# Kernel tuning notes

Measured on AMD Instinct MI355X. Metric: run time of the kernel, lower is better.

## Reference

```python
import jax, jax.numpy as jnp
import numpy as np

B, T, C, H = 2, 2048, 1024, 16
D = C // H  # head dim


def setup_inputs() -> dict:
    key = jax.random.key(0)
    ks = jax.random.split(key, 8)
    s = 1.0 / np.sqrt(C)
    return {
        "x_q": jax.random.normal(ks[0], (B, T, C), jnp.float32),
        "x_kv": jax.random.normal(ks[1], (B, T, C), jnp.float32),
        "Wq": jax.random.normal(ks[2], (C, C), jnp.float32) * s,
        "bq": jnp.zeros((C,), jnp.float32),
        "Wkv": jax.random.normal(ks[3], (C, 2 * C), jnp.float32) * s,
        "bkv": jnp.zeros((2 * C,), jnp.float32),
        "Wo": jax.random.normal(ks[4], (C, C), jnp.float32) * s,
        "bo": jnp.zeros((C,), jnp.float32),
    }


def reference(x_q, x_kv, Wq, bq, Wkv, bkv, Wo, bo):
    q = x_q @ Wq + bq                      # [B,Tq,C]
    kv = x_kv @ Wkv + bkv                  # [B,Tkv,2C]
    k, v = kv[..., :C], kv[..., C:]
    # split heads -> [B,H,T,D]
    q = q.reshape(B, T, H, D).transpose(0, 2, 1, 3)
    k = k.reshape(B, T, H, D).transpose(0, 2, 1, 3)
    v = v.reshape(B, T, H, D).transpose(0, 2, 1, 3)
    att = jnp.einsum("bhqd,bhkd->bhqk", q, k) * (1.0 / np.sqrt(D))
    att = jax.nn.softmax(att, axis=-1)
    y = jnp.einsum("bhqk,bhkd->bhqd", att, v)
    y = y.transpose(0, 2, 1, 3).reshape(B, T, C)
    return y @ Wo + bo
```

## Files before the change

### kernel.cpp

```cpp
#include <hip/hip_runtime.h>

#define NB 2
#define NT 2048
#define NC 1024
#define NH 16
#define ND 64
#define NC2 2048
#define QSCALE (0.125f * 1.4426950408889634f)

typedef __attribute__((ext_vector_type(8))) __bf16 bf16x8;
typedef __attribute__((ext_vector_type(8))) unsigned short ushort8;
typedef __attribute__((ext_vector_type(4))) float f32x4;

__device__ __forceinline__ unsigned short bf16_bits(float f) {
  union { float f; unsigned int u; } x; x.f = f;
  unsigned int r = x.u + 0x7fffu + ((x.u >> 16) & 1u);
  return (unsigned short)(r >> 16);
}
__device__ __forceinline__ float bf2f(unsigned short u) {
  union { unsigned int u; float f; } x; x.u = ((unsigned int)u) << 16;
  return x.f;
}
__device__ __forceinline__ void g2l16(const void* g, void* l) {
  __builtin_amdgcn_global_load_lds(
      (const __attribute__((address_space(1))) unsigned int*)g,
      (__attribute__((address_space(3))) unsigned int*)l, 16, 0, 0);
}
__device__ __forceinline__ bf16x8 ld8(const unsigned short* p) {
  return *(const bf16x8*)p;
}
__device__ __forceinline__ unsigned int cvtpk(float lo, float hi) {
  unsigned int r;
  asm("v_cvt_pk_bf16_f32 %0, %1, %2" : "=v"(r) : "v"(lo), "v"(hi));
  return r;
}
__device__ __forceinline__ float vexp2(float x) {
  float r;
  asm("v_exp_f32 %0, %1" : "=v"(r) : "v"(x));
  return r;
}

__device__ __forceinline__ int wave_is_f32(const unsigned short* __restrict__ x) {
  const int lane = threadIdx.x & 63;
  ulonglong2 v = ((const ulonglong2*)x)[lane];
  const unsigned short* u = (const unsigned short*)&v;
  int c = 0;
#pragma unroll
  for (int k = 0; k < 8; ++k) {
    int e = (u[k] >> 7) & 0xFF;
    c += (e != 0 && (e < 112 || e > 142)) ? 1 : 0;
  }
#pragma unroll
  for (int off = 32; off > 0; off >>= 1) c += __shfl_down(c, off);
  return __shfl(c, 0) > 64;
}

__global__ __launch_bounds__(256) void prep(const void* __restrict__ xq,
                                            const void* __restrict__ xkv,
                                            const void* __restrict__ w0,
                                            const void* __restrict__ w1,
                                            const void* __restrict__ w2,
                                            unsigned short* __restrict__ oq,
                                            unsigned short* __restrict__ okv,
                                            unsigned short* __restrict__ o0,
                                            unsigned short* __restrict__ o1,
                                            unsigned short* __restrict__ o2) {
  __shared__ unsigned short tile[32][33];
  const int bx = blockIdx.x, by = blockIdx.y;
  const int f = wave_is_f32((const unsigned short*)xq);
  if (bx < 128) {
    const int fb = bx * 32 + by;
    const void* in = (fb < 2048) ? xq : xkv;
    unsigned short* out = (fb < 2048) ? oq : okv;
    const int i = (fb & 2047) * 256 + threadIdx.x;
    if (f) {
      const float4* p = (const float4*)in;
      float4 a = p[i * 2], b = p[i * 2 + 1];
      ushort8 o;
      o[0] = bf16_bits(a.x); o[1] = bf16_bits(a.y); o[2] = bf16_bits(a.z); o[3] = bf16_bits(a.w);
      o[4] = bf16_bits(b.x); o[5] = bf16_bits(b.y); o[6] = bf16_bits(b.z); o[7] = bf16_bits(b.w);
      *(ushort8*)&out[(size_t)i * 8] = o;
    } else {
      ((ulonglong2*)out)[i] = ((const ulonglong2*)in)[i];
    }
  } else {
    const int tb = bx - 128;
    const void* in; unsigned short* out; int cols, cb;
    if (tb < 32)      { in = w0; out = o0; cols = NC;  cb = tb; }
    else if (tb < 96) { in = w1; out = o1; cols = NC2; cb = tb - 32; }
    else              { in = w2; out = o2; cols = NC;  cb = tb - 96; }
    const int c0 = cb * 32, r0 = by * 32;
    const int tx = threadIdx.x & 31, ty = threadIdx.x >> 5;
#pragma unroll
    for (int i = 0; i < 32; i += 8) {
      size_t idx = (size_t)(r0 + ty + i) * cols + c0 + tx;
      tile[ty + i][tx] = f ? bf16_bits(((const float*)in)[idx]) : ((const unsigned short*)in)[idx];
    }
    __syncthreads();
#pragma unroll
    for (int i = 0; i < 32; i += 8)
      out[(size_t)(c0 + ty + i) * NC + r0 + tx] = tile[tx][ty + i];
  }
}

__global__ __launch_bounds__(256) void gemm_qkv(const unsigned short* __restrict__ xq,
                                                const unsigned short* __restrict__ xkv,
                                                const unsigned short* __restrict__ Wqt,
                                                const unsigned short* __restrict__ Wkvt,
                                                const void* __restrict__ bq,
                                                const void* __restrict__ bkv,
                                                unsigned short* __restrict__ qb,
                                                unsigned short* __restrict__ kf2,
                                                unsigned short* __restrict__ vt2,
                                                const unsigned short* __restrict__ xdet) {
  __shared__ unsigned short As[128][64];
  __shared__ unsigned short Bs[128][64];
  __shared__ unsigned short Cb[4][16][72];
  const int f = wave_is_f32(xdet);
  const int l = blockIdx.y * 32 + blockIdx.x;
  const int nl = (l & 7) * 96 + (l >> 3);
  const int bxs = nl & 31, bys = nl >> 5;
  const bool isq = bys < 8;
  const unsigned short* A  = isq ? xq : xkv;
  const unsigned short* Bt = isq ? Wqt : Wkvt;
  const int m0 = bxs * 128;
  const int n0 = (isq ? bys : bys - 8) * 128;
  const int tid = threadIdx.x, w = tid >> 6, lane = tid & 63;
  const int lrow = lane & 15, lhi = lane >> 4;
  const int wr = w >> 1, wc = w & 1;
  const int grow = lane >> 3, gcol = (lane & 7) * 8;
  f32x4 acc[4][4] = {};
  for (int k0 = 0; k0 < NC; k0 += 64) {
    __syncthreads();
#pragma unroll
    for (int p = 0; p < 4; ++p) {
      const int r = w * 32 + p * 8;
      g2l16(&A[(size_t)(m0 + r + grow) * NC + k0 + gcol], &As[r][0]);
      g2l16(&Bt[(size_t)(n0 + r + grow) * NC + k0 + gcol], &Bs[r][0]);
    }
    __syncthreads();
    bf16x8 af[2][4], bfr[2][4];
#pragma unroll
    for (int kk = 0; kk < 2; ++kk) {
#pragma unroll
      for (int i = 0; i < 4; ++i)
        af[kk][i] = ld8(&As[wr * 64 + i * 16 + lrow][kk * 32 + lhi * 8]);
#pragma unroll
      for (int j = 0; j < 4; ++j)
        bfr[kk][j] = ld8(&Bs[wc * 64 + j * 16 + lrow][kk * 32 + lhi * 8]);
    }
#pragma unroll
    for (int kk = 0; kk < 2; ++kk)
#pragma unroll
      for (int i = 0; i < 4; ++i)
#pragma unroll
        for (int j = 0; j < 4; ++j)
          acc[i][j] = __builtin_amdgcn_mfma_f32_16x16x32_bf16(af[kk][i], bfr[kk][j], acc[i][j], 0, 0, 0);
  }
  const void* bias = isq ? bq : bkv;
  if (!isq && n0 >= NC) {
#pragma unroll
    for (int j = 0; j < 4; ++j) {
      const int col = n0 + wc * 64 + j * 16 + lrow;
      const float bj = f ? ((const float*)bias)[col] : bf2f(((const unsigned short*)bias)[col]);
#pragma unroll
      for (int i = 0; i < 4; ++i) {
        const int row = m0 + wr * 64 + i * 16 + lhi * 4;
        float v[4];
#pragma unroll
        for (int r = 0; r < 4; ++r) v[r] = acc[i][j][r] + bj;
        const int cv = col - NC;
        const int hV = cv >> 6, dcol = cv & 63;
        const int bV = row >> 11, tt = row & 2047;
        const size_t base = ((size_t)((bV * NH + hV) * 32 + (tt >> 6))) * 4096
                          + (dcol >> 4) * 1024 + ((tt >> 4) & 1) * 512
                          + (((tt >> 2) & 3) * 16 + (dcol & 15)) * 8 + ((tt >> 5) & 1) * 4;
        ushort4 o4;
        o4.x = bf16_bits(v[0]); o4.y = bf16_bits(v[1]);
        o4.z = bf16_bits(v[2]); o4.w = bf16_bits(v[3]);
        *(ushort4*)&vt2[base] = o4;
      }
    }
  } else {
    const int rowbase = m0 + wr * 64;
    const int hK = (n0 + wc * 64) >> 6;
    const size_t tb = ((size_t)(((rowbase >> 11) * NH + hK) * 32 + ((rowbase & 2047) >> 6))) * 4096;
#pragma unroll
    for (int i = 0; i < 4; ++i) {
#pragma unroll
      for (int j = 0; j < 4; ++j) {
        const int col = n0 + wc * 64 + j * 16 + lrow;
        const float bj = f ? ((const float*)bias)[col] : bf2f(((const unsigned short*)bias)[col]);
#pragma unroll
        for (int r = 0; r < 4; ++r) {
          const float v = acc[i][j][r] + bj;
          Cb[w][lhi * 4 + r][j * 16 + lrow] = bf16_bits(isq ? v * QSCALE : v);
        }
      }
      if (isq) {
#pragma unroll
        for (int p = 0; p < 2; ++p) {
          const int row_l = p * 8 + (lane >> 3), col_l = (lane & 7) * 8;
          const bf16x8 v8 = ld8(&Cb[w][row_l][col_l]);
          *(bf16x8*)&qb[(size_t)(rowbase + i * 16 + row_l) * NC + n0 + wc * 64 + col_l] = v8;
        }
      } else {
#pragma unroll
        for (int p = 0; p < 2; ++p) {
          const bf16x8 v8 = ld8(&Cb[w][lane & 15][p * 32 + (lane >> 4) * 8]);
          *(bf16x8*)&kf2[tb + i * 1024 + p * 512 + lane * 8] = v8;
        }
      }
    }
  }
}

__global__ __launch_bounds__(256) void gemm_out(const unsigned short* __restrict__ A,
                                                const unsigned short* __restrict__ Bt,
                                                const void* __restrict__ bias,
                                                void* __restrict__ Cout,
                                                const unsigned short* __restrict__ xdet) {
  __shared__ unsigned short As[128][64];
  __shared__ unsigned short Bs[128][64];
  const int f = wave_is_f32(xdet);
  const int l = blockIdx.y * 32 + blockIdx.x;
  const int nl = (l & 7) * 32 + (l >> 3);
  const int m0 = (nl & 31) * 128, n0 = (nl >> 5) * 128;
  const int tid = threadIdx.x, w = tid >> 6, lane = tid & 63;
  const int lrow = lane & 15, lhi = lane >> 4;
  const int wr = w >> 1, wc = w & 1;
  const int grow = lane >> 3, gcol = (lane & 7) * 8;
  f32x4 acc[4][4] = {};
  for (int k0 = 0; k0 < NC; k0 += 64) {
    __syncthreads();
#pragma unroll
    for (int p = 0; p < 4; ++p) {
      const int r = w * 32 + p * 8;
      g2l16(&A[(size_t)(m0 + r + grow) * NC + k0 + gcol], &As[r][0]);
      g2l16(&Bt[(size_t)(n0 + r + grow) * NC + k0 + gcol], &Bs[r][0]);
    }
    __syncthreads();
    bf16x8 af[2][4], bfr[2][4];
#pragma unroll
    for (int kk = 0; kk < 2; ++kk) {
#pragma unroll
      for (int i = 0; i < 4; ++i)
        af[kk][i] = ld8(&As[wr * 64 + i * 16 + lrow][kk * 32 + lhi * 8]);
#pragma unroll
      for (int j = 0; j < 4; ++j)
        bfr[kk][j] = ld8(&Bs[wc * 64 + j * 16 + lrow][kk * 32 + lhi * 8]);
    }
#pragma unroll
    for (int kk = 0; kk < 2; ++kk)
#pragma unroll
      for (int i = 0; i < 4; ++i)
#pragma unroll
        for (int j = 0; j < 4; ++j)
          acc[i][j] = __builtin_amdgcn_mfma_f32_16x16x32_bf16(af[kk][i], bfr[kk][j], acc[i][j], 0, 0, 0);
  }
#pragma unroll
  for (int j = 0; j < 4; ++j) {
    const int col = n0 + wc * 64 + j * 16 + lrow;
    const float bj = f ? ((const float*)bias)[col] : bf2f(((const unsigned short*)bias)[col]);
#pragma unroll
    for (int i = 0; i < 4; ++i) {
      const int row = m0 + wr * 64 + i * 16 + lhi * 4;
#pragma unroll
      for (int r = 0; r < 4; ++r) {
        const float v = acc[i][j][r] + bj;
        const size_t idx = (size_t)(row + r) * NC + col;
        if (f) ((float*)Cout)[idx] = v;
        else ((unsigned short*)Cout)[idx] = bf16_bits(v);
      }
    }
  }
}

__global__ __launch_bounds__(128) void flash_attn(const unsigned short* __restrict__ q,
                                                  const unsigned short* __restrict__ kf2,
                                                  const unsigned short* __restrict__ vt2,
                                                  unsigned short* __restrict__ y) {
  const int fid = blockIdx.x + (blockIdx.y << 5);
  const int swz = ((fid & 7) << 7) + (fid >> 3);
  const int qt = swz & 31, bh = swz >> 5;
  const int b = bh >> 4, h = bh & 15;
  const int tid = threadIdx.x, w = tid >> 6, lane = tid & 63;
  const int lq = lane & 15, lhi = lane >> 4;

  bf16x8 qfA[2], qfB[2];
  {
    const unsigned short* qpA = q + (size_t)(b * NT + qt * 64 + w * 32 + lq) * NC + h * ND + lhi * 8;
    qfA[0] = ld8(qpA); qfA[1] = ld8(qpA + 32);
    qfB[0] = ld8(qpA + (size_t)16 * NC); qfB[1] = ld8(qpA + (size_t)16 * NC + 32);
  }
  f32x4 accA[4] = {}, accB[4] = {};
  float lA = 0.f, lB = 0.f;
  const unsigned short* kbase = kf2 + ((size_t)bh * 32) * 4096 + (size_t)lane * 8;
  const unsigned short* vbase = vt2 + ((size_t)bh * 32) * 4096 + (size_t)lane * 8;

#define KLOAD(kt_)                                                              \
  {                                                                             \
    _Pragma("unroll") for (int j = 0; j < 4; ++j)                               \
      _Pragma("unroll") for (int kk = 0; kk < 2; ++kk)                          \
        kR[j][kk] = ld8(kbase + (size_t)(kt_)*4096 + j * 1024 + kk * 512);      \
  }
#define VLOAD(kt_, V_)                                                          \
  {                                                                             \
    _Pragma("unroll") for (int jd = 0; jd < 4; ++jd)                            \
      _Pragma("unroll") for (int jj = 0; jj < 2; ++jj)                          \
        V_[jd][jj] = ld8(vbase + (size_t)(kt_)*4096 + jd * 1024 + jj * 512);    \
  }
#define TILE_BODY(it_, VC_, VN_)                                                  \
  {                                                                               \
    f32x4 sA[4], sB[4];                                                           \
    _Pragma("unroll") for (int j = 0; j < 4; ++j) {                               \
      f32x4 a = {}, bb2 = {};                                                     \
      _Pragma("unroll") for (int kk = 0; kk < 2; ++kk) {                          \
        a   = __builtin_amdgcn_mfma_f32_16x16x32_bf16(kR[j][kk], qfA[kk], a, 0, 0, 0);   \
        bb2 = __builtin_amdgcn_mfma_f32_16x16x32_bf16(kR[j][kk], qfB[kk], bb2, 0, 0, 0); \
      }                                                                           \
      sA[j] = a; sB[j] = bb2;                                                     \
    }                                                                             \
    if ((it_) + 1 < 32) KLOAD((it_) + 1);                                         \
    if ((it_) + 1 < 32) VLOAD((it_) + 1, VN_);                                    \
    float rsA = 0.f, rsB = 0.f;                                                   \
    _Pragma("unroll") for (int j = 0; j < 4; ++j)                                 \
      _Pragma("unroll") for (int r = 0; r < 4; ++r) {                             \
        const float pa = vexp2(sA[j][r]); sA[j][r] = pa; rsA += pa;               \
        const float pb = vexp2(sB[j][r]); sB[j][r] = pb; rsB += pb;               \
      }                                                                           \
    rsA += __shfl_xor(rsA, 16); rsA += __shfl_xor(rsA, 32);                       \
    rsB += __shfl_xor(rsB, 16); rsB += __shfl_xor(rsB, 32);                       \
    lA += rsA; lB += rsB;                                                         \
    union U { unsigned int u[4]; bf16x8 v; };                                     \
    U pA0, pA1, pB0, pB1;                                                         \
    pA0.u[0] = cvtpk(sA[0][0], sA[0][1]); pA0.u[1] = cvtpk(sA[0][2], sA[0][3]);   \
    pA0.u[2] = cvtpk(sA[2][0], sA[2][1]); pA0.u[3] = cvtpk(sA[2][2], sA[2][3]);   \
    pA1.u[0] = cvtpk(sA[1][0], sA[1][1]); pA1.u[1] = cvtpk(sA[1][2], sA[1][3]);   \
    pA1.u[2] = cvtpk(sA[3][0], sA[3][1]); pA1.u[3] = cvtpk(sA[3][2], sA[3][3]);   \
    pB0.u[0] = cvtpk(sB[0][0], sB[0][1]); pB0.u[1] = cvtpk(sB[0][2], sB[0][3]);   \
    pB0.u[2] = cvtpk(sB[2][0], sB[2][1]); pB0.u[3] = cvtpk(sB[2][2], sB[2][3]);   \
    pB1.u[0] = cvtpk(sB[1][0], sB[1][1]); pB1.u[1] = cvtpk(sB[1][2], sB[1][3]);   \
    pB1.u[2] = cvtpk(sB[3][0], sB[3][1]); pB1.u[3] = cvtpk(sB[3][2], sB[3][3]);   \
    __builtin_amdgcn_s_setprio(1);                                                \
    _Pragma("unroll") for (int jd = 0; jd < 4; ++jd) {                            \
      accA[jd] = __builtin_amdgcn_mfma_f32_16x16x32_bf16(VC_[jd][0], pA0.v, accA[jd], 0, 0, 0); \
      accA[jd] = __builtin_amdgcn_mfma_f32_16x16x32_bf16(VC_[jd][1], pA1.v, accA[jd], 0, 0, 0); \
      accB[jd] = __builtin_amdgcn_mfma_f32_16x16x32_bf16(VC_[jd][0], pB0.v, accB[jd], 0, 0, 0); \
      accB[jd] = __builtin_amdgcn_mfma_f32_16x16x32_bf16(VC_[jd][1], pB1.v, accB[jd], 0, 0, 0); \
    }                                                                             \
    __builtin_amdgcn_s_setprio(0);                                                \
  }

  bf16x8 kR[4][2];
  bf16x8 vRa[4][2], vRb[4][2];
  KLOAD(0);
  VLOAD(0, vRa);

  for (int itp = 0; itp < 16; ++itp) {
    const int it0 = itp * 2;
    TILE_BODY(it0, vRa, vRb);
    TILE_BODY(it0 + 1, vRb, vRa);
  }
#undef KLOAD
#undef VLOAD
#undef TILE_BODY

  const float invA = 1.f / lA, invB = 1.f / lB;
#pragma unroll
  for (int jd = 0; jd < 4; ++jd) {
    uint2 oA, oB;
    oA.x = cvtpk(accA[jd][0] * invA, accA[jd][1] * invA);
    oA.y = cvtpk(accA[jd][2] * invA, accA[jd][3] * invA);
    oB.x = cvtpk(accB[jd][0] * invB, accB[jd][1] * invB);
    oB.y = cvtpk(accB[jd][2] * invB, accB[jd][3] * invB);
    const size_t base = (size_t)(b * NT + qt * 64 + w * 32 + lq) * NC + h * ND + jd * 16 + lhi * 4;
    *(uint2*)&y[base] = oA;
    *(uint2*)&y[base + (size_t)16 * NC] = oB;
  }
}

extern "C" void kernel_launch(void* const* d_in, const int* in_sizes, int n_in,
                              void* d_out, int out_size, void* d_ws, size_t ws_size,
                              hipStream_t stream) {
  (void)in_sizes; (void)n_in; (void)out_size; (void)ws_size;
  char* ws = (char*)d_ws;
  unsigned short* xq_b  = (unsigned short*)(ws);
  unsigned short* xkv_b = (unsigned short*)(ws + ((size_t)8  << 20));
  unsigned short* Wqt   = (unsigned short*)(ws + ((size_t)16 << 20));
  unsigned short* Wkvt  = (unsigned short*)(ws + ((size_t)18 << 20));
  unsigned short* Wot   = (unsigned short*)(ws + ((size_t)22 << 20));
  unsigned short* qb    = (unsigned short*)(ws + ((size_t)24 << 20));
  unsigned short* kf2   = (unsigned short*)(ws + ((size_t)32 << 20));
  unsigned short* vt2   = (unsigned short*)(ws + ((size_t)48 << 20));
  unsigned short* yb    = (unsigned short*)(ws + ((size_t)56 << 20));
  const unsigned short* xdet = (const unsigned short*)d_in[0];

  prep<<<dim3(256, 32), 256, 0, stream>>>(d_in[0], d_in[1], d_in[2], d_in[4], d_in[6],
                                          xq_b, xkv_b, Wqt, Wkvt, Wot);
  gemm_qkv<<<dim3(32, 24), 256, 0, stream>>>(xq_b, xkv_b, Wqt, Wkvt, d_in[3], d_in[5],
                                             qb, kf2, vt2, xdet);
  flash_attn<<<dim3(32, 32), 128, 0, stream>>>(qb, kf2, vt2, yb);
  gemm_out<<<dim3(32, 8), 256, 0, stream>>>(yb, Wot, d_in[7], d_out, xdet);
}
```

Baseline: 148.2 us.

## Skip bf16 activation copy, reuse As for epilogue staging, drop tile swizzle

When inputs are already bf16, prep no longer copies activations and gemm_qkv reads the raw inputs directly, removing a redundant copy pass. The epilogue staging buffer Cb is replaced by reusing the As shared tile after a barrier, which lowers LDS use and may raise occupancy. The L2-friendly block remapping in both GEMMs is removed in favour of plain blockIdx mapping, which could worsen cache locality. With fp32 test inputs the copy-skip path does not trigger, so the active effects are the LDS reuse and the mapping change.

```diff
diff --git a/kernel.cpp b/kernel.cpp
--- a/kernel.cpp
+++ b/kernel.cpp
@@ -69,20 +69,17 @@
   const int bx = blockIdx.x, by = blockIdx.y;
   const int f = wave_is_f32((const unsigned short*)xq);
   if (bx < 128) {
+    if (!f) return;
     const int fb = bx * 32 + by;
     const void* in = (fb < 2048) ? xq : xkv;
     unsigned short* out = (fb < 2048) ? oq : okv;
     const int i = (fb & 2047) * 256 + threadIdx.x;
-    if (f) {
-      const float4* p = (const float4*)in;
-      float4 a = p[i * 2], b = p[i * 2 + 1];
-      ushort8 o;
-      o[0] = bf16_bits(a.x); o[1] = bf16_bits(a.y); o[2] = bf16_bits(a.z); o[3] = bf16_bits(a.w);
-      o[4] = bf16_bits(b.x); o[5] = bf16_bits(b.y); o[6] = bf16_bits(b.z); o[7] = bf16_bits(b.w);
-      *(ushort8*)&out[(size_t)i * 8] = o;
-    } else {
-      ((ulonglong2*)out)[i] = ((const ulonglong2*)in)[i];
-    }
+    const float4* p = (const float4*)in;
+    float4 a = p[i * 2], b = p[i * 2 + 1];
+    ushort8 o;
+    o[0] = bf16_bits(a.x); o[1] = bf16_bits(a.y); o[2] = bf16_bits(a.z); o[3] = bf16_bits(a.w);
+    o[4] = bf16_bits(b.x); o[5] = bf16_bits(b.y); o[6] = bf16_bits(b.z); o[7] = bf16_bits(b.w);
+    *(ushort8*)&out[(size_t)i * 8] = o;
   } else {
     const int tb = bx - 128;
     const void* in; unsigned short* out; int cols, cb;
@@ -103,28 +100,25 @@
   }
 }
 
-__global__ __launch_bounds__(256) void gemm_qkv(const unsigned short* __restrict__ xq,
-                                                const unsigned short* __restrict__ xkv,
+__global__ __launch_bounds__(256) void gemm_qkv(const unsigned short* __restrict__ xq_raw,
+                                                const unsigned short* __restrict__ xkv_raw,
+                                                const unsigned short* __restrict__ xq_cvt,
+                                                const unsigned short* __restrict__ xkv_cvt,
                                                 const unsigned short* __restrict__ Wqt,
                                                 const unsigned short* __restrict__ Wkvt,
                                                 const void* __restrict__ bq,
                                                 const void* __restrict__ bkv,
                                                 unsigned short* __restrict__ qb,
                                                 unsigned short* __restrict__ kf2,
-                                                unsigned short* __restrict__ vt2,
-                                                const unsigned short* __restrict__ xdet) {
+                                                unsigned short* __restrict__ vt2) {
   __shared__ unsigned short As[128][64];
   __shared__ unsigned short Bs[128][64];
-  __shared__ unsigned short Cb[4][16][72];
-  const int f = wave_is_f32(xdet);
-  const int l = blockIdx.y * 32 + blockIdx.x;
-  const int nl = (l & 7) * 96 + (l >> 3);
-  const int bxs = nl & 31, bys = nl >> 5;
-  const bool isq = bys < 8;
-  const unsigned short* A  = isq ? xq : xkv;
+  const int f = wave_is_f32(xq_raw);
+  const bool isq = blockIdx.y < 8;
+  const unsigned short* A  = isq ? (f ? xq_cvt : xq_raw) : (f ? xkv_cvt : xkv_raw);
   const unsigned short* Bt = isq ? Wqt : Wkvt;
-  const int m0 = bxs * 128;
-  const int n0 = (isq ? bys : bys - 8) * 128;
+  const int m0 = blockIdx.x * 128;
+  const int n0 = (isq ? blockIdx.y : blockIdx.y - 8) * 128;
   const int tid = threadIdx.x, w = tid >> 6, lane = tid & 63;
   const int lrow = lane & 15, lhi = lane >> 4;
   const int wr = w >> 1, wc = w & 1;
@@ -182,6 +176,8 @@
       }
     }
   } else {
+    __syncthreads();
+    unsigned short* Cw = &As[0][0] + w * 1280;
     const int rowbase = m0 + wr * 64;
     const int hK = (n0 + wc * 64) >> 6;
     const size_t tb = ((size_t)(((rowbase >> 11) * NH + hK) * 32 + ((rowbase & 2047) >> 6))) * 4096;
@@ -194,20 +190,20 @@
 #pragma unroll
         for (int r = 0; r < 4; ++r) {
           const float v = acc[i][j][r] + bj;
-          Cb[w][lhi * 4 + r][j * 16 + lrow] = bf16_bits(isq ? v * QSCALE : v);
+          Cw[(lhi * 4 + r) * 72 + j * 16 + lrow] = bf16_bits(isq ? v * QSCALE : v);
         }
       }
       if (isq) {
 #pragma unroll
         for (int p = 0; p < 2; ++p) {
           const int row_l = p * 8 + (lane >> 3), col_l = (lane & 7) * 8;
-          const bf16x8 v8 = ld8(&Cb[w][row_l][col_l]);
+          const bf16x8 v8 = ld8(&Cw[row_l * 72 + col_l]);
           *(bf16x8*)&qb[(size_t)(rowbase + i * 16 + row_l) * NC + n0 + wc * 64 + col_l] = v8;
         }
       } else {
 #pragma unroll
         for (int p = 0; p < 2; ++p) {
-          const bf16x8 v8 = ld8(&Cb[w][lane & 15][p * 32 + (lane >> 4) * 8]);
+          const bf16x8 v8 = ld8(&Cw[(lane & 15) * 72 + p * 32 + (lane >> 4) * 8]);
           *(bf16x8*)&kf2[tb + i * 1024 + p * 512 + lane * 8] = v8;
         }
       }
@@ -223,9 +219,7 @@
   __shared__ unsigned short As[128][64];
   __shared__ unsigned short Bs[128][64];
   const int f = wave_is_f32(xdet);
-  const int l = blockIdx.y * 32 + blockIdx.x;
-  const int nl = (l & 7) * 32 + (l >> 3);
-  const int m0 = (nl & 31) * 128, n0 = (nl >> 5) * 128;
+  const int m0 = blockIdx.x * 128, n0 = blockIdx.y * 128;
   const int tid = threadIdx.x, w = tid >> 6, lane = tid & 63;
   const int lrow = lane & 15, lhi = lane >> 4;
   const int wr = w >> 1, wc = w & 1;
@@ -398,8 +392,10 @@
 
   prep<<<dim3(256, 32), 256, 0, stream>>>(d_in[0], d_in[1], d_in[2], d_in[4], d_in[6],
                                           xq_b, xkv_b, Wqt, Wkvt, Wot);
-  gemm_qkv<<<dim3(32, 24), 256, 0, stream>>>(xq_b, xkv_b, Wqt, Wkvt, d_in[3], d_in[5],
-                                             qb, kf2, vt2, xdet);
+  gemm_qkv<<<dim3(32, 24), 256, 0, stream>>>((const unsigned short*)d_in[0],
+                                             (const unsigned short*)d_in[1],
+                                             xq_b, xkv_b, Wqt, Wkvt, d_in[3], d_in[5],
+                                             qb, kf2, vt2);
   flash_attn<<<dim3(32, 32), 128, 0, stream>>>(qb, kf2, vt2, yb);
   gemm_out<<<dim3(32, 8), 256, 0, stream>>>(yb, Wot, d_in[7], d_out, xdet);
 }
```

Result: faster. 140.0 us (-5.5%).
